# Kernel optimization log

Measured on AMD Instinct MI355X. Metric: run time of the kernel, lower is better.

Reference implementation:

```python
import jax, jax.numpy as jnp
import numpy as np

EPS = 1e-12  # F.normalize eps

def _l2norm(x):
    n = jnp.linalg.norm(x, axis=-1, keepdims=True)
    return x / jnp.maximum(n, EPS)

def setup_inputs() -> dict:
    key = jax.random.key(0)
    k1, k2, k3, k4 = jax.random.split(key, 4)
    N, D = 16384, 256
    img = jax.random.normal(k1, (N, D), dtype=jnp.float32)
    txt = jax.random.normal(k2, (N, D), dtype=jnp.float32)
    t_prime = jax.random.normal(k3, (), dtype=jnp.float32)
    bias = jax.random.normal(k4, (), dtype=jnp.float32)
    return {"img": img, "txt": txt, "t_prime": t_prime, "bias": bias}

def reference(img, txt, t_prime, bias):
    # world_size == 1 path of DistributedSigLoss.forward
    n = img.shape[0]
    image_features = _l2norm(img)
    text_features = _l2norm(txt)
    # logits = exp(t') * img @ txt.T + b   -> [N, N]
    logits = jnp.exp(t_prime) * (image_features @ text_features.T) + bias
    # labels = 2*I - 1 (positive pairs on the diagonal, negatives elsewhere)
    labels = 2.0 * jnp.eye(n, dtype=logits.dtype) - 1.0
    loss = -jnp.sum(jax.nn.log_sigmoid(labels * logits)) / n
    return loss
```

## Files before the change

### kernel.cpp

```cpp
#include <hip/hip_runtime.h>

typedef int   i32x4 __attribute__((ext_vector_type(4)));
typedef int   i32x8 __attribute__((ext_vector_type(8)));
typedef float f32x16 __attribute__((ext_vector_type(16)));

#define D_DIM 256
#define LOG2E 1.4426950408889634f
#define LN2   0.6931471805599453f
#define STRIP_BYTES 32768
#define NBLK 16384

#if __has_builtin(__builtin_amdgcn_exp2f)
static __device__ __forceinline__ float exp2_fast(float x) { return __builtin_amdgcn_exp2f(x); }
#else
static __device__ __forceinline__ float exp2_fast(float x) { return __expf(x * LN2); }
#endif
#if __has_builtin(__builtin_amdgcn_logf)
static __device__ __forceinline__ float log2_fast(float x) { return __builtin_amdgcn_logf(x); }
#else
static __device__ __forceinline__ float log2_fast(float x) { return __logf(x) * LOG2E; }
#endif

#if __has_builtin(__builtin_amdgcn_cvt_pk_fp8_f32)
static __device__ __forceinline__ unsigned int pack4_fp8(float a, float b, float c, float d) {
    int v = 0;
    v = __builtin_amdgcn_cvt_pk_fp8_f32(a, b, v, false);
    v = __builtin_amdgcn_cvt_pk_fp8_f32(c, d, v, true);
    return (unsigned int)v;
}
#else
#include <hip/hip_fp8.h>
static __device__ __forceinline__ unsigned char cv1(float x) {
    __hip_fp8_e4m3 f(x);
    union { __hip_fp8_e4m3 f; unsigned char b; } u; u.f = f; return u.b;
}
static __device__ __forceinline__ unsigned int pack4_fp8(float a, float b, float c, float d) {
    return (unsigned int)cv1(a) | ((unsigned int)cv1(b) << 8) |
           ((unsigned int)cv1(c) << 16) | ((unsigned int)cv1(d) << 24);
}
#endif

static __device__ __forceinline__ f32x16 mfma_fp8_32x32_k64(i32x8 a, i32x8 b, f32x16 c) {
#if __has_builtin(__builtin_amdgcn_mfma_scale_f32_32x32x64_f8f6f4)
    return __builtin_amdgcn_mfma_scale_f32_32x32x64_f8f6f4(a, b, c, 0, 0, 0, 127, 0, 127);
#else
    union { i32x8 v; long l[4]; } ua, ub;
    ua.v = a; ub.v = b;
#pragma unroll
    for (int s = 0; s < 4; ++s)
        c = __builtin_amdgcn_mfma_f32_32x32x16_fp8_fp8(ua.l[s], ub.l[s], c, 0, 0, 0);
    return c;
#endif
}

__global__ __launch_bounds__(256) void norm_cast_kernel(
    const float* __restrict__ img, const float* __restrict__ txt,
    unsigned char* __restrict__ Ab, unsigned char* __restrict__ Bb, int N)
{
    const int wave = threadIdx.x >> 6;
    const int lane = threadIdx.x & 63;
    int gRow = blockIdx.x * 4 + wave;

    const float* src;
    unsigned char* dstB;
    int row;
    if (gRow < N) { row = gRow;     src = img + (size_t)row * D_DIM; dstB = Ab; }
    else          { row = gRow - N; src = txt + (size_t)row * D_DIM; dstB = Bb; }

    float4 v = ((const float4*)src)[lane];
    float ss = v.x*v.x + v.y*v.y + v.z*v.z + v.w*v.w;
#pragma unroll
    for (int off = 1; off < 64; off <<= 1)
        ss += __shfl_xor(ss, off, 64);
    float inv = 1.0f / fmaxf(sqrtf(ss), 1e-12f);

    unsigned int w = pack4_fp8(v.x*inv, v.y*inv, v.z*inv, v.w*inv);
    unsigned char* dst = dstB + (size_t)(row >> 7) * STRIP_BYTES
                       + (lane >> 2) * 2048 + (row & 127) * 16 + (lane & 3) * 4;
    *(unsigned int*)dst = w;
}

__global__ __launch_bounds__(256, 4) void siglip_loss_kernel(
    const unsigned char* __restrict__ A, const unsigned char* __restrict__ B,
    const float* __restrict__ t_prime, const float* __restrict__ bias,
    float* __restrict__ partials, int N)
{
    __shared__ unsigned char As[2][8192];
    __shared__ unsigned char Bs[2][8192];
    __shared__ float red[4];

    const int tid  = threadIdx.x;
    const int wave = tid >> 6;
    const int lane = tid & 63;
    const int r31  = lane & 31;
    const int g    = lane >> 5;
    const int wv   = wave >> 1;
    const int wu   = wave & 1;

    const int bid = blockIdx.x;
    const int st  = bid >> 8;
    const int l2  = bid & 255;
    const int bx  = (st & 7) * 16 + (l2 & 15);
    const int by  = (st >> 3) * 16 + (l2 >> 4);
    const int rowBase = by * 128;
    const int colBase = bx * 128;

    const unsigned char* Astrip = A + (size_t)by * STRIP_BYTES;
    const unsigned char* Bstrip = B + (size_t)bx * STRIP_BYTES;

    auto stage = [&](int buf, int c) {
        const unsigned char* ga = Astrip + c * 8192;
        const unsigned char* gb = Bstrip + c * 8192;
#pragma unroll
        for (int l = 0; l < 2; ++l) {
            int idx = wave * 2 + l;
            __builtin_amdgcn_global_load_lds(
                (const __attribute__((address_space(1))) unsigned int*)(ga + idx * 1024 + lane * 16),
                (__attribute__((address_space(3))) unsigned int*)&As[buf][idx * 1024],
                16, 0, 0);
            __builtin_amdgcn_global_load_lds(
                (const __attribute__((address_space(1))) unsigned int*)(gb + idx * 1024 + lane * 16),
                (__attribute__((address_space(3))) unsigned int*)&Bs[buf][idx * 1024],
                16, 0, 0);
        }
    };

    stage(0, 0);

    int a_off[2], b_off[2];
#pragma unroll
    for (int i = 0; i < 2; ++i) a_off[i] = g * 4096 + (wv * 64 + i * 32 + r31) * 16;
#pragma unroll
    for (int j = 0; j < 2; ++j) b_off[j] = g * 4096 + (wu * 64 + j * 32 + r31) * 16;

    f32x16 acc[2][2] = {};
    union F { i32x8 v8; i32x4 v4[2]; };

#pragma unroll 1
    for (int c = 0; c < 4; ++c) {
        __syncthreads();
        if (c < 3) stage((c + 1) & 1, c + 1);

        const unsigned char* as = As[c & 1];
        const unsigned char* bs = Bs[c & 1];
        F a[2], b[2];
#pragma unroll
        for (int i = 0; i < 2; ++i) {
            a[i].v4[0] = *(const i32x4*)&as[a_off[i]];
            a[i].v4[1] = *(const i32x4*)&as[a_off[i] + 2048];
            b[i].v4[0] = *(const i32x4*)&bs[b_off[i]];
            b[i].v4[1] = *(const i32x4*)&bs[b_off[i] + 2048];
        }
#pragma unroll
        for (int i = 0; i < 2; ++i)
#pragma unroll
            for (int j = 0; j < 2; ++j)
                acc[i][j] = mfma_fp8_32x32_k64(a[i].v8, b[j].v8, acc[i][j]);
    }

    const float s2 = __expf(t_prime[0]) * LOG2E;
    const float b2 = bias[0] * LOG2E;
    float local = 0.0f;
#pragma unroll
    for (int i = 0; i < 2; ++i)
#pragma unroll
        for (int j = 0; j < 2; ++j)
#pragma unroll
            for (int g2 = 0; g2 < 2; ++g2) {
                float x[8];
#pragma unroll
                for (int e = 0; e < 8; ++e)
                    x[e] = exp2_fast(fmaf(s2, acc[i][j][g2 * 8 + e], b2));
                float p = 1.0f + x[0];
#pragma unroll
                for (int e = 1; e < 8; ++e)
                    p = fmaf(p, x[e], p);
                local += log2_fast(p);
            }

    if (rowBase == colBase) {
#pragma unroll
        for (int i = 0; i < 2; ++i)
#pragma unroll
            for (int j = 0; j < 2; ++j)
#pragma unroll
                for (int r = 0; r < 16; ++r) {
                    int rowf = (r & 3) + 8 * (r >> 2) + 4 * g;
                    int grow = wv * 64 + i * 32 + rowf;
                    int gcol = wu * 64 + j * 32 + r31;
                    if (grow == gcol) local -= fmaf(s2, acc[i][j][r], b2);
                }
    }

#pragma unroll
    for (int off = 32; off > 0; off >>= 1)
        local += __shfl_xor(local, off, 64);
    if (lane == 0) red[wave] = local;
    __syncthreads();
    if (tid == 0)
        partials[bid] = (red[0] + red[1]) + (red[2] + red[3]);
}

__global__ __launch_bounds__(1024) void reduce_kernel(
    const float* __restrict__ partials, float* __restrict__ out, int N)
{
    __shared__ float red[16];
    const int tid  = threadIdx.x;
    const int wave = tid >> 6;
    const int lane = tid & 63;
    float s = 0.0f;
#pragma unroll 4
    for (int i = tid; i < NBLK; i += 1024)
        s += partials[i];
#pragma unroll
    for (int off = 32; off > 0; off >>= 1)
        s += __shfl_xor(s, off, 64);
    if (lane == 0) red[wave] = s;
    __syncthreads();
    if (tid == 0) {
        float t = 0.0f;
#pragma unroll
        for (int w = 0; w < 16; ++w) t += red[w];
        out[0] = t * (LN2 / (float)N);
    }
}

extern "C" void kernel_launch(void* const* d_in, const int* in_sizes, int n_in,
                              void* d_out, int out_size, void* d_ws, size_t ws_size,
                              hipStream_t stream) {
    const float* img = (const float*)d_in[0];
    const float* txt = (const float*)d_in[1];
    const float* tp  = (const float*)d_in[2];
    const float* bs  = (const float*)d_in[3];
    float* out = (float*)d_out;
    int N = in_sizes[0] / D_DIM;

    unsigned char* Ab = (unsigned char*)d_ws;
    unsigned char* Bb = Ab + (size_t)N * D_DIM;
    float* partials   = (float*)(Bb + (size_t)N * D_DIM);

    norm_cast_kernel<<<(2 * N) / 4, 256, 0, stream>>>(img, txt, Ab, Bb, N);
    siglip_loss_kernel<<<NBLK, 256, 0, stream>>>(Ab, Bb, tp, bs, partials, N);
    reduce_kernel<<<1, 1024, 0, stream>>>(partials, out, N);
}
```

Baseline: 168.5 us.

## Enlarge loss kernel tile to 256x256 with 8 waves per block

```diff
diff --git a/kernel.cpp b/kernel.cpp
--- a/kernel.cpp
+++ b/kernel.cpp
@@ -8,7 +8,7 @@
 #define LOG2E 1.4426950408889634f
 #define LN2   0.6931471805599453f
 #define STRIP_BYTES 32768
-#define NBLK 16384
+#define GRID2 4096
 
 #if __has_builtin(__builtin_amdgcn_exp2f)
 static __device__ __forceinline__ float exp2_fast(float x) { return __builtin_amdgcn_exp2f(x); }
@@ -80,60 +80,66 @@
     *(unsigned int*)dst = w;
 }
 
-__global__ __launch_bounds__(256, 4) void siglip_loss_kernel(
+__global__ __launch_bounds__(512, 2) void siglip_loss_kernel(
     const unsigned char* __restrict__ A, const unsigned char* __restrict__ B,
     const float* __restrict__ t_prime, const float* __restrict__ bias,
     float* __restrict__ partials, int N)
 {
-    __shared__ unsigned char As[2][8192];
-    __shared__ unsigned char Bs[2][8192];
-    __shared__ float red[4];
+    __shared__ unsigned char As[2][16384];
+    __shared__ unsigned char Bs[2][16384];
+    __shared__ float red[8];
 
     const int tid  = threadIdx.x;
     const int wave = tid >> 6;
     const int lane = tid & 63;
     const int r31  = lane & 31;
     const int g    = lane >> 5;
-    const int wv   = wave >> 1;
-    const int wu   = wave & 1;
+    const int wm   = wave >> 2;
+    const int wn   = wave & 3;
 
     const int bid = blockIdx.x;
-    const int st  = bid >> 8;
-    const int l2  = bid & 255;
-    const int bx  = (st & 7) * 16 + (l2 & 15);
-    const int by  = (st >> 3) * 16 + (l2 >> 4);
-    const int rowBase = by * 128;
-    const int colBase = bx * 128;
-
-    const unsigned char* Astrip = A + (size_t)by * STRIP_BYTES;
-    const unsigned char* Bstrip = B + (size_t)bx * STRIP_BYTES;
+    const int st  = bid >> 6;
+    const int l2  = bid & 63;
+    const int bx  = (st & 7) * 8 + (l2 & 7);
+    const int by  = (st >> 3) * 8 + (l2 >> 3);
 
     auto stage = [&](int buf, int c) {
-        const unsigned char* ga = Astrip + c * 8192;
-        const unsigned char* gb = Bstrip + c * 8192;
-#pragma unroll
-        for (int l = 0; l < 2; ++l) {
-            int idx = wave * 2 + l;
-            __builtin_amdgcn_global_load_lds(
-                (const __attribute__((address_space(1))) unsigned int*)(ga + idx * 1024 + lane * 16),
-                (__attribute__((address_space(3))) unsigned int*)&As[buf][idx * 1024],
-                16, 0, 0);
-            __builtin_amdgcn_global_load_lds(
-                (const __attribute__((address_space(1))) unsigned int*)(gb + idx * 1024 + lane * 16),
-                (__attribute__((address_space(3))) unsigned int*)&Bs[buf][idx * 1024],
-                16, 0, 0);
+#pragma unroll
+        for (int li = 0; li < 4; ++li) {
+            int l = wave * 4 + li;
+            int lb = l & 15;
+            int kcl   = lb >> 2;
+            int half  = (lb >> 1) & 1;
+            int inner = (lb & 1) * 1024;
+            if (l < 16) {
+                const unsigned char* src = A + (size_t)(2 * by + half) * STRIP_BYTES
+                                         + (4 * c + kcl) * 2048 + inner + lane * 16;
+                __builtin_amdgcn_global_load_lds(
+                    (const __attribute__((address_space(1))) unsigned int*)src,
+                    (__attribute__((address_space(3))) unsigned int*)&As[buf][l * 1024],
+                    16, 0, 0);
+            } else {
+                const unsigned char* src = B + (size_t)(2 * bx + half) * STRIP_BYTES
+                                         + (4 * c + kcl) * 2048 + inner + lane * 16;
+                __builtin_amdgcn_global_load_lds(
+                    (const __attribute__((address_space(1))) unsigned int*)src,
+                    (__attribute__((address_space(3))) unsigned int*)&Bs[buf][lb * 1024],
+                    16, 0, 0);
+            }
         }
     };
 
     stage(0, 0);
 
-    int a_off[2], b_off[2];
-#pragma unroll
-    for (int i = 0; i < 2; ++i) a_off[i] = g * 4096 + (wv * 64 + i * 32 + r31) * 16;
-#pragma unroll
-    for (int j = 0; j < 2; ++j) b_off[j] = g * 4096 + (wu * 64 + j * 32 + r31) * 16;
-
-    f32x16 acc[2][2] = {};
+    int a_off[4], b_off[2];
+#pragma unroll
+    for (int i = 0; i < 4; ++i)
+        a_off[i] = g * 8192 + wm * 2048 + (i * 32 + r31) * 16;
+#pragma unroll
+    for (int j = 0; j < 2; ++j)
+        b_off[j] = g * 8192 + (wn >> 1) * 2048 + ((wn & 1) * 64 + j * 32 + r31) * 16;
+
+    f32x16 acc[4][2] = {};
     union F { i32x8 v8; i32x4 v4[2]; };
 
 #pragma unroll 1
@@ -143,26 +149,31 @@
 
         const unsigned char* as = As[c & 1];
         const unsigned char* bs = Bs[c & 1];
-        F a[2], b[2];
-#pragma unroll
-        for (int i = 0; i < 2; ++i) {
+        F a[4], b[2];
+#pragma unroll
+        for (int j = 0; j < 2; ++j) {
+            b[j].v4[0] = *(const i32x4*)&bs[b_off[j]];
+            b[j].v4[1] = *(const i32x4*)&bs[b_off[j] + 4096];
+        }
+#pragma unroll
+        for (int i = 0; i < 4; ++i) {
             a[i].v4[0] = *(const i32x4*)&as[a_off[i]];
-            a[i].v4[1] = *(const i32x4*)&as[a_off[i] + 2048];
-            b[i].v4[0] = *(const i32x4*)&bs[b_off[i]];
-            b[i].v4[1] = *(const i32x4*)&bs[b_off[i] + 2048];
+            a[i].v4[1] = *(const i32x4*)&as[a_off[i] + 4096];
         }
-#pragma unroll
-        for (int i = 0; i < 2; ++i)
+        __builtin_amdgcn_s_setprio(1);
+#pragma unroll
+        for (int i = 0; i < 4; ++i)
 #pragma unroll
             for (int j = 0; j < 2; ++j)
                 acc[i][j] = mfma_fp8_32x32_k64(a[i].v8, b[j].v8, acc[i][j]);
+        __builtin_amdgcn_s_setprio(0);
     }
 
     const float s2 = __expf(t_prime[0]) * LOG2E;
     const float b2 = bias[0] * LOG2E;
     float local = 0.0f;
 #pragma unroll
-    for (int i = 0; i < 2; ++i)
+    for (int i = 0; i < 4; ++i)
 #pragma unroll
         for (int j = 0; j < 2; ++j)
 #pragma unroll
@@ -178,16 +189,16 @@
                 local += log2_fast(p);
             }
 
-    if (rowBase == colBase) {
-#pragma unroll
-        for (int i = 0; i < 2; ++i)
+    if (by == bx) {
+#pragma unroll
+        for (int i = 0; i < 4; ++i)
 #pragma unroll
             for (int j = 0; j < 2; ++j)
 #pragma unroll
                 for (int r = 0; r < 16; ++r) {
                     int rowf = (r & 3) + 8 * (r >> 2) + 4 * g;
-                    int grow = wv * 64 + i * 32 + rowf;
-                    int gcol = wu * 64 + j * 32 + r31;
+                    int grow = wm * 128 + i * 32 + rowf;
+                    int gcol = wn * 64 + j * 32 + r31;
                     if (grow == gcol) local -= fmaf(s2, acc[i][j][r], b2);
                 }
     }
@@ -197,8 +208,12 @@
         local += __shfl_xor(local, off, 64);
     if (lane == 0) red[wave] = local;
     __syncthreads();
-    if (tid == 0)
-        partials[bid] = (red[0] + red[1]) + (red[2] + red[3]);
+    if (tid == 0) {
+        float t = 0.0f;
+#pragma unroll
+        for (int w = 0; w < 8; ++w) t += red[w];
+        partials[bid] = t;
+    }
 }
 
 __global__ __launch_bounds__(1024) void reduce_kernel(
@@ -210,7 +225,7 @@
     const int lane = tid & 63;
     float s = 0.0f;
 #pragma unroll 4
-    for (int i = tid; i < NBLK; i += 1024)
+    for (int i = tid; i < GRID2; i += 1024)
         s += partials[i];
 #pragma unroll
     for (int off = 32; off > 0; off >>= 1)
@@ -240,6 +255,6 @@
     float* partials   = (float*)(Bb + (size_t)N * D_DIM);
 
     norm_cast_kernel<<<(2 * N) / 4, 256, 0, stream>>>(img, txt, Ab, Bb, N);
-    siglip_loss_kernel<<<NBLK, 256, 0, stream>>>(Ab, Bb, tp, bs, partials, N);
+    siglip_loss_kernel<<<GRID2, 512, 0, stream>>>(Ab, Bb, tp, bs, partials, N);
     reduce_kernel<<<1, 1024, 0, stream>>>(partials, out, N);
 }
```

After: 179.4 us. 6.5% more time.
